# Optimization experiments

Measured on AMD Instinct MI355X. Metric: run time of the kernel, lower is better.

The kernel has to match this reference:

```python
import jax, jax.numpy as jnp
import numpy as np

N = 20000        # nodes
E = 320000       # edges (avg degree 16)
F_IN = 128       # node_features
F2 = 64          # second_features (per-head out dim, LSTM hidden)
H = 8            # heads
D1 = H * F2      # 512, concat output of GATConv / LSTM input
NEG_SLOPE = 0.2  # GATConv default leaky_relu slope


def _gat_conv(x, src, dst, W, att_src, att_dst, bias):
    """PyG GATConv (concat=True, self-loops added, eval-mode dropout)."""
    n = x.shape[0]
    h = (x @ W).reshape(n, H, -1)                      # [N,H,F]
    a_s = (h * att_src).sum(-1)                        # [N,H]
    a_d = (h * att_dst).sum(-1)                        # [N,H]
    e = jax.nn.leaky_relu(a_s[src] + a_d[dst], NEG_SLOPE)   # [E',H]
    m = jax.ops.segment_max(e, dst, num_segments=n)    # [N,H]
    m = jnp.where(jnp.isfinite(m), m, 0.0)
    ex = jnp.exp(e - m[dst])
    denom = jax.ops.segment_sum(ex, dst, num_segments=n)
    alpha = ex / (denom[dst] + 1e-16)                  # [E',H]
    msg = h[src] * alpha[:, :, None]                   # [E',H,F]
    out = jax.ops.segment_sum(msg, dst, num_segments=n)  # [N,H,F]
    return out.reshape(n, -1) + bias                   # [N,H*F]


def _lstm_step(x, W_ih, W_hh, b_ih, b_hh):
    """Single-timestep PyTorch LSTM with zero initial (h0, c0). x: [N,D1]."""
    h0 = jnp.zeros((x.shape[0], F2), x.dtype)
    gates = x @ W_ih.T + b_ih + h0 @ W_hh.T + b_hh     # [N,4*F2]
    i, f, g, o = jnp.split(gates, 4, axis=-1)
    c = jax.nn.sigmoid(f) * 0.0 + jax.nn.sigmoid(i) * jnp.tanh(g)
    h = jax.nn.sigmoid(o) * jnp.tanh(c)
    return h, (h, c)


def setup_inputs() -> dict:
    key = jax.random.key(0)
    ks = jax.random.split(key, 16)

    def glorot(k, shape, fan_in):
        return jax.random.normal(k, shape, jnp.float32) * (1.0 / np.sqrt(fan_in))

    return {
        "x": jax.random.normal(ks[0], (N, F_IN), jnp.float32),
        "edge_index": jax.random.randint(ks[1], (2, E), 0, N, jnp.int32),
        "edge_weight": jax.random.uniform(ks[2], (E,), jnp.float32),
        # GATConv 1: F_IN -> H*F2
        "W1": glorot(ks[3], (F_IN, H * F2), F_IN),
        "att_src1": glorot(ks[4], (H, F2), F2),
        "att_dst1": glorot(ks[5], (H, F2), F2),
        "bias1": jnp.zeros((H * F2,), jnp.float32),
        # LSTM: input D1 -> hidden F2
        "W_ih": glorot(ks[6], (4 * F2, D1), D1),
        "W_hh": glorot(ks[7], (4 * F2, F2), F2),
        "b_ih": jnp.zeros((4 * F2,), jnp.float32),
        "b_hh": jnp.zeros((4 * F2,), jnp.float32),
        # GATConv 2: F2 -> H*F2
        "W2": glorot(ks[8], (F2, H * F2), F2),
        "att_src2": glorot(ks[9], (H, F2), F2),
        "att_dst2": glorot(ks[10], (H, F2), F2),
        "bias2": jnp.zeros((H * F2,), jnp.float32),
    }


def reference(x, edge_index, edge_weight, W1, att_src1, att_dst1, bias1,
              W_ih, W_hh, b_ih, b_hh, W2, att_src2, att_dst2, bias2):
    # edge_weight is accepted but unused, matching the original forward.
    loops = jnp.arange(N, dtype=edge_index.dtype)
    src = jnp.concatenate([edge_index[0], loops])      # add self-loops (PyG default)
    dst = jnp.concatenate([edge_index[1], loops])

    h = _gat_conv(x, src, dst, W1, att_src1, att_dst1, bias1)   # [N,512]
    h, hidden2 = _lstm_step(h, W_ih, W_hh, b_ih, b_hh)          # [N,64]
    h = jax.nn.relu(h)
    h = _gat_conv(h, src, dst, W2, att_src2, att_dst2, bias2)   # [N,512]
    return jax.nn.softmax(h, axis=1)
```

## Files before the change

kernel.cpp:

```cpp
#include <hip/hip_runtime.h>
#include <math.h>
#include <stdint.h>


__global__ void count_kernel(const int* __restrict__ dst, int* __restrict__ deg, int E) {
  int i = blockIdx.x * 256 + threadIdx.x;
  if (i < E) atomicAdd(&deg[dst[i]], 1);
}

__global__ void scan_kernel(const int* __restrict__ deg, int* __restrict__ rowptr, int n) {
  __shared__ int buf[1024];
  const int tid = threadIdx.x;
  const int i0 = tid * 20;
  int v[20];
  int tsum = 0;
#pragma unroll
  for (int k = 0; k < 20; ++k) {
    int i = i0 + k;
    v[k] = (i < n) ? (deg[i] + 1) : 0;
    tsum += v[k];
  }
  int incl = tsum;
  buf[tid] = incl;
  __syncthreads();
  for (int s = 1; s < 1024; s <<= 1) {
    int t = (tid >= (unsigned)s) ? buf[tid - s] : 0;
    __syncthreads();
    incl += t;
    buf[tid] = incl;
    __syncthreads();
  }
  int excl = incl - tsum;
#pragma unroll
  for (int k = 0; k < 20; ++k) {
    int i = i0 + k;
    if (i < n) rowptr[i] = excl;
    excl += v[k];
  }
  if (tid == 1023) rowptr[n] = incl;
}

__global__ void scatter_kernel(const int* __restrict__ src, const int* __restrict__ dst,
                               const int* __restrict__ rowptr, int* __restrict__ wp,
                               int* __restrict__ col, int E, int n) {
  int i = blockIdx.x * 256 + threadIdx.x;
  if (i < E) {
    int d = dst[i];
    int p = rowptr[d] + atomicAdd(&wp[d], 1);
    col[p] = src[i];
  } else if (i < E + n) {
    int d = i - E;
    int p = rowptr[d] + atomicAdd(&wp[d], 1);
    col[p] = d;
  }
}


__device__ __forceinline__ uint16_t bf16r(float x) {
  uint32_t u = __float_as_uint(x);
  return (uint16_t)((u + 0x7FFFu + ((u >> 16) & 1u)) >> 16);
}
__device__ __forceinline__ void bfsplit(float x, uint16_t& h, uint16_t& l) {
  h = bf16r(x);
  float hf = __uint_as_float((uint32_t)h << 16);
  l = bf16r(x - hf);
}

using bf16x8 = __attribute__((ext_vector_type(8))) short;
using f32x4  = __attribute__((ext_vector_type(4))) float;


__global__ __launch_bounds__(256) void gemm_mfma(
    const float* __restrict__ A, const uint16_t* __restrict__ Bh,
    const uint16_t* __restrict__ Bl, float* __restrict__ C,
    const float* __restrict__ bias,
    int M, int K, int lda, int aZ, int bZ, int ldc, int cZ, int biasZ) {
  constexpr int BM = 128, BN = 64, BK = 64;
  __shared__ __align__(16) uint16_t sAh[BM * BK], sAl[BM * BK];
  __shared__ __align__(16) uint16_t sBh[BN * BK], sBl[BN * BK];
  const int z = blockIdx.z;
  A += (size_t)z * aZ;
  Bh += (size_t)z * bZ;
  Bl += (size_t)z * bZ;
  C += (size_t)z * cZ;
  const int tid = threadIdx.x;
  const int wid = tid >> 6, lane = tid & 63;
  const int bm = blockIdx.y * BM;
  const int bn = blockIdx.x * BN;
  const int fr = lane & 15;
  const int kg = lane >> 4;
  const int mbase = wid * 32;
  f32x4 acc[2][4] = {};

  for (int k0 = 0; k0 < K; k0 += BK) {
#pragma unroll
    for (int s = 0; s < 8; ++s) {
      int idx = tid + s * 256;
      int row = idx >> 4;
      int c4 = (idx & 15) * 4;
      float4 v = make_float4(0.f, 0.f, 0.f, 0.f);
      if (bm + row < M)
        v = *reinterpret_cast<const float4*>(A + (size_t)(bm + row) * lda + k0 + c4);
      ushort4 h, l;
      bfsplit(v.x, h.x, l.x); bfsplit(v.y, h.y, l.y);
      bfsplit(v.z, h.z, l.z); bfsplit(v.w, h.w, l.w);
      int off = (row * BK + c4) * 2;
      off ^= (row & 7) << 4;
      *reinterpret_cast<ushort4*>(reinterpret_cast<char*>(sAh) + off) = h;
      *reinterpret_cast<ushort4*>(reinterpret_cast<char*>(sAl) + off) = l;
    }
#pragma unroll
    for (int s = 0; s < 2; ++s) {
      int idx = tid + s * 256;
      int row = idx >> 3;
      int c8 = (idx & 7) * 8;
      uint4 vh = *reinterpret_cast<const uint4*>(Bh + (size_t)(bn + row) * K + k0 + c8);
      uint4 vl = *reinterpret_cast<const uint4*>(Bl + (size_t)(bn + row) * K + k0 + c8);
      int off = (row * BK + c8) * 2;
      off ^= (row & 7) << 4;
      *reinterpret_cast<uint4*>(reinterpret_cast<char*>(sBh) + off) = vh;
      *reinterpret_cast<uint4*>(reinterpret_cast<char*>(sBl) + off) = vl;
    }
    __syncthreads();
#pragma unroll
    for (int ks = 0; ks < 2; ++ks) {
      bf16x8 ah[2], al[2], bh[4], bl[4];
#pragma unroll
      for (int i = 0; i < 2; ++i) {
        int m = mbase + i * 16 + fr;
        int off = m * (BK * 2) + ks * 64 + kg * 16;
        off ^= (m & 7) << 4;
        ah[i] = *reinterpret_cast<const bf16x8*>(reinterpret_cast<const char*>(sAh) + off);
        al[i] = *reinterpret_cast<const bf16x8*>(reinterpret_cast<const char*>(sAl) + off);
      }
#pragma unroll
      for (int j = 0; j < 4; ++j) {
        int n = j * 16 + fr;
        int off = n * (BK * 2) + ks * 64 + kg * 16;
        off ^= (n & 7) << 4;
        bh[j] = *reinterpret_cast<const bf16x8*>(reinterpret_cast<const char*>(sBh) + off);
        bl[j] = *reinterpret_cast<const bf16x8*>(reinterpret_cast<const char*>(sBl) + off);
      }
#pragma unroll
      for (int i = 0; i < 2; ++i)
#pragma unroll
        for (int j = 0; j < 4; ++j) {
          acc[i][j] = __builtin_amdgcn_mfma_f32_16x16x32_bf16(ah[i], bh[j], acc[i][j], 0, 0, 0);
          acc[i][j] = __builtin_amdgcn_mfma_f32_16x16x32_bf16(al[i], bh[j], acc[i][j], 0, 0, 0);
          acc[i][j] = __builtin_amdgcn_mfma_f32_16x16x32_bf16(ah[i], bl[j], acc[i][j], 0, 0, 0);
        }
    }
    __syncthreads();
  }
  float bz[4];
#pragma unroll
  for (int j = 0; j < 4; ++j)
    bz[j] = bias ? bias[(size_t)z * biasZ + bn + j * 16 + fr] : 0.f;
#pragma unroll
  for (int i = 0; i < 2; ++i) {
    int mr = bm + mbase + i * 16 + kg * 4;
#pragma unroll
    for (int r = 0; r < 4; ++r) {
      int m = mr + r;
      if (m < M) {
#pragma unroll
        for (int j = 0; j < 4; ++j)
          C[(size_t)m * ldc + bn + j * 16 + fr] = acc[i][j][r] + bz[j];
      }
    }
  }
}


__global__ void prep_all_kernel(const float* __restrict__ W_ih, const float* __restrict__ b_ih,
                                const float* __restrict__ b_hh, const float* __restrict__ W1,
                                const float* __restrict__ as1, const float* __restrict__ ad1,
                                const float* __restrict__ W2, const float* __restrict__ as2,
                                const float* __restrict__ ad2,
                                int* __restrict__ degwp,
                                uint16_t* __restrict__ Wtbh, uint16_t* __restrict__ Wtbl,
                                uint16_t* __restrict__ Bt1h, uint16_t* __restrict__ Bt1l,
                                uint16_t* __restrict__ Bt2h, uint16_t* __restrict__ Bt2l,
                                float* __restrict__ bsum, float* __restrict__ watt1,
                                float* __restrict__ watt2, int n2) {
  int idx = blockIdx.x * 256 + threadIdx.x;
  if (idx < n2) {
    degwp[idx] = 0;
    return;
  }
  int t = idx - n2;
  if (t < 98304) {
    int jp = t >> 9, k = t & 511;
    int j = (jp < 64) ? jp : jp + 64;
    uint16_t h, l;
    bfsplit(W_ih[(size_t)j * 512 + k], h, l);
    Wtbh[t] = h; Wtbl[t] = l;
    return;
  }
  t -= 98304;
  if (t < 65536) {
    int n = t >> 7, k = t & 127;
    uint16_t h, l;
    bfsplit(W1[(size_t)k * 512 + n], h, l);
    Bt1h[t] = h; Bt1l[t] = l;
    return;
  }
  t -= 65536;
  if (t < 32768) {
    int n = t >> 6, k = t & 63;
    uint16_t h, l;
    bfsplit(W2[(size_t)k * 512 + n], h, l);
    Bt2h[t] = h; Bt2l[t] = l;
    return;
  }
  t -= 32768;
  if (t < 192) {
    int j = (t < 64) ? t : t + 64;
    bsum[t] = b_ih[j] + b_hh[j];
    return;
  }
  t -= 192;
  if (t < 2048) {
    int f = t >> 4, c = t & 15;
    int k = c & 7;
    const float* att = ((c < 8) ? as1 : ad1) + k * 64;
    const float* w = W1 + (size_t)f * 512 + k * 64;
    float s = 0.f;
#pragma unroll
    for (int j = 0; j < 64; ++j) s = fmaf(w[j], att[j], s);
    watt1[t] = s;
    return;
  }
  t -= 2048;
  if (t < 1024) {
    int f = t >> 4, c = t & 15;
    int k = c & 7;
    const float* att = ((c < 8) ? as2 : ad2) + k * 64;
    const float* w = W2 + (size_t)f * 512 + k * 64;
    float s = 0.f;
#pragma unroll
    for (int j = 0; j < 64; ++j) s = fmaf(w[j], att[j], s);
    watt2[t] = s;
  }
}


template <int F>
__global__ __launch_bounds__(256) void attcoef_kernel(
    const float* __restrict__ feat, const float* __restrict__ watt,
    float* __restrict__ a_s, float* __restrict__ a_d, int n) {
  __shared__ float rows[16 * F];
  __shared__ float wbuf[F * 16];
  const int n0 = blockIdx.x * 16;
  const int tid = threadIdx.x;
  if (n0 + 16 <= n) {
    const float4* g = reinterpret_cast<const float4*>(feat + (size_t)n0 * F);
    float4* l = reinterpret_cast<float4*>(rows);
    for (int i = tid; i < 16 * F / 4; i += 256) l[i] = g[i];
  } else {
    for (int i = tid; i < 16 * F; i += 256) {
      int r = i / F;
      rows[i] = (n0 + r < n) ? feat[(size_t)(n0 + r) * F + (i - r * F)] : 0.f;
    }
  }
  {
    const float4* g = reinterpret_cast<const float4*>(watt);
    float4* l = reinterpret_cast<float4*>(wbuf);
    for (int i = tid; i < F * 16 / 4; i += 256) l[i] = g[i];
  }
  __syncthreads();
  const int local = tid >> 4, c = tid & 15;
  float s = 0.f;
#pragma unroll 8
  for (int f = 0; f < F; ++f) s = fmaf(rows[local * F + f], wbuf[f * 16 + c], s);
  const int node = n0 + local;
  if (node < n) {
    if (c < 8) a_s[(size_t)node * 8 + c] = s;
    else       a_d[(size_t)node * 8 + (c - 8)] = s;
  }
}


template <int F>
__global__ __launch_bounds__(256) void gat_aggregate_wave(
    const float* __restrict__ feat, const float* __restrict__ a_s,
    const float* __restrict__ a_d, const int* __restrict__ rowptr,
    const int* __restrict__ col, float* __restrict__ agg, int n) {
  constexpr int F4 = F / 4;
  constexpr int HPG = (F == 128) ? 4 : 2;
  __shared__ float s_alpha[4][8][8];
  __shared__ int s_cols[4][8];
  const int wid = threadIdx.x >> 6;
  const int lane = threadIdx.x & 63;
  const int node = blockIdx.x * 4 + wid;
  if (node >= n) return;
  const int start = rowptr[node];
  const int deg = rowptr[node + 1] - start;
  const int j = lane >> 3;
  const int h = lane & 7;
  const float adh = a_d[(size_t)node * 8 + h];
  float den = 0.f;
  for (int e = j; e < deg; e += 8) {
    int s = col[start + e];
    float v = a_s[(size_t)s * 8 + h] + adh;
    v = (v > 0.f) ? v : 0.2f * v;
    den += __expf(v);
  }
  den += __shfl_xor(den, 8);
  den += __shfl_xor(den, 16);
  den += __shfl_xor(den, 32);
  const float inv = 1.f / (den + 1e-16f);
  const int f4 = lane & (F4 - 1);
  const int hbase = (lane / F4) * HPG;
  float4 acc0 = make_float4(0.f, 0.f, 0.f, 0.f);
  float4 acc1 = make_float4(0.f, 0.f, 0.f, 0.f);
  float4 acc2 = make_float4(0.f, 0.f, 0.f, 0.f);
  float4 acc3 = make_float4(0.f, 0.f, 0.f, 0.f);
  for (int c0 = 0; c0 < deg; c0 += 8) {
    float aval = 0.f;
    int sj = 0;
    if (c0 + j < deg) {
      sj = col[start + c0 + j];
      float v = a_s[(size_t)sj * 8 + h] + adh;
      v = (v > 0.f) ? v : 0.2f * v;
      aval = __expf(v) * inv;
    }
    s_alpha[wid][j][h] = aval;
    if (h == 0) s_cols[wid][j] = sj;
    __builtin_amdgcn_wave_barrier();
    const int ce = min(8, deg - c0);
    for (int e = 0; e < ce; ++e) {
      int s = s_cols[wid][e];
      float4 fv = *reinterpret_cast<const float4*>(feat + (size_t)s * F + f4 * 4);
      if constexpr (HPG == 4) {
        float4 al = *reinterpret_cast<const float4*>(&s_alpha[wid][e][hbase]);
        acc0.x = fmaf(al.x, fv.x, acc0.x); acc0.y = fmaf(al.x, fv.y, acc0.y);
        acc0.z = fmaf(al.x, fv.z, acc0.z); acc0.w = fmaf(al.x, fv.w, acc0.w);
        acc1.x = fmaf(al.y, fv.x, acc1.x); acc1.y = fmaf(al.y, fv.y, acc1.y);
        acc1.z = fmaf(al.y, fv.z, acc1.z); acc1.w = fmaf(al.y, fv.w, acc1.w);
        acc2.x = fmaf(al.z, fv.x, acc2.x); acc2.y = fmaf(al.z, fv.y, acc2.y);
        acc2.z = fmaf(al.z, fv.z, acc2.z); acc2.w = fmaf(al.z, fv.w, acc2.w);
        acc3.x = fmaf(al.w, fv.x, acc3.x); acc3.y = fmaf(al.w, fv.y, acc3.y);
        acc3.z = fmaf(al.w, fv.z, acc3.z); acc3.w = fmaf(al.w, fv.w, acc3.w);
      } else {
        float2 al = *reinterpret_cast<const float2*>(&s_alpha[wid][e][hbase]);
        acc0.x = fmaf(al.x, fv.x, acc0.x); acc0.y = fmaf(al.x, fv.y, acc0.y);
        acc0.z = fmaf(al.x, fv.z, acc0.z); acc0.w = fmaf(al.x, fv.w, acc0.w);
        acc1.x = fmaf(al.y, fv.x, acc1.x); acc1.y = fmaf(al.y, fv.y, acc1.y);
        acc1.z = fmaf(al.y, fv.z, acc1.z); acc1.w = fmaf(al.y, fv.w, acc1.w);
      }
    }
    __builtin_amdgcn_wave_barrier();
  }
  float* outp = agg + (size_t)node * 8 * F + (size_t)hbase * F + f4 * 4;
  *reinterpret_cast<float4*>(outp) = acc0;
  *reinterpret_cast<float4*>(outp + F) = acc1;
  if constexpr (HPG == 4) {
    *reinterpret_cast<float4*>(outp + 2 * F) = acc2;
    *reinterpret_cast<float4*>(outp + 3 * F) = acc3;
  }
}


__global__ __launch_bounds__(256) void lstm_act_attcoef_kernel(
    const float* __restrict__ gates, const float* __restrict__ bsum,
    const float* __restrict__ watt2, float* __restrict__ h2,
    float* __restrict__ a_s2, float* __restrict__ a_d2, int n) {
  __shared__ float h2t[4][64];
  __shared__ float wbuf[64 * 16];
  const int tid = threadIdx.x;
  reinterpret_cast<float4*>(wbuf)[tid] = reinterpret_cast<const float4*>(watt2)[tid];
  const int nl = tid >> 6, j = tid & 63;
  const int node = blockIdx.x * 4 + nl;
  float hv = 0.f;
  if (node < n) {
    const float* g0 = gates + (size_t)node * 192;
    float iv = g0[j] + bsum[j];
    float gv = g0[64 + j] + bsum[64 + j];
    float ov = g0[128 + j] + bsum[128 + j];
    float c = (1.f / (1.f + __expf(-iv))) * tanhf(gv);
    hv = fmaxf((1.f / (1.f + __expf(-ov))) * tanhf(c), 0.f);
    h2[(size_t)node * 64 + j] = hv;
  }
  h2t[nl][j] = hv;
  __syncthreads();
  if (j < 16 && node < n) {
    float s = 0.f;
#pragma unroll 16
    for (int f = 0; f < 64; ++f) s = fmaf(h2t[nl][f], wbuf[f * 16 + j], s);
    if (j < 8) a_s2[(size_t)node * 8 + j] = s;
    else       a_d2[(size_t)node * 8 + (j - 8)] = s;
  }
}


__global__ __launch_bounds__(256) void softmax512_wave(const float* __restrict__ in,
                                                       float* __restrict__ out, int n) {
  const int wid = threadIdx.x >> 6, lane = threadIdx.x & 63;
  const int node = blockIdx.x * 4 + wid;
  if (node >= n) return;
  const float4* ip = reinterpret_cast<const float4*>(in + (size_t)node * 512);
  float4 v0 = ip[lane];
  float4 v1 = ip[64 + lane];
  float m = fmaxf(fmaxf(fmaxf(v0.x, v0.y), fmaxf(v0.z, v0.w)),
                  fmaxf(fmaxf(v1.x, v1.y), fmaxf(v1.z, v1.w)));
#pragma unroll
  for (int d = 1; d < 64; d <<= 1) m = fmaxf(m, __shfl_xor(m, d));
  float4 e0, e1;
  e0.x = __expf(v0.x - m); e0.y = __expf(v0.y - m);
  e0.z = __expf(v0.z - m); e0.w = __expf(v0.w - m);
  e1.x = __expf(v1.x - m); e1.y = __expf(v1.y - m);
  e1.z = __expf(v1.z - m); e1.w = __expf(v1.w - m);
  float s = e0.x + e0.y + e0.z + e0.w + e1.x + e1.y + e1.z + e1.w;
#pragma unroll
  for (int d = 1; d < 64; d <<= 1) s += __shfl_xor(s, d);
  float inv = 1.f / s;
  e0.x *= inv; e0.y *= inv; e0.z *= inv; e0.w *= inv;
  e1.x *= inv; e1.y *= inv; e1.z *= inv; e1.w *= inv;
  float4* op = reinterpret_cast<float4*>(out + (size_t)node * 512);
  op[lane] = e0;
  op[64 + lane] = e1;
}


extern "C" void kernel_launch(void* const* d_in, const int* in_sizes, int n_in,
                              void* d_out, int out_size, void* d_ws, size_t ws_size,
                              hipStream_t stream) {
  const float* x      = (const float*)d_in[0];
  const int*   ei     = (const int*)d_in[1];
  const float* W1     = (const float*)d_in[3];
  const float* att_s1 = (const float*)d_in[4];
  const float* att_d1 = (const float*)d_in[5];
  const float* bias1  = (const float*)d_in[6];
  const float* W_ih   = (const float*)d_in[7];
  const float* b_ih   = (const float*)d_in[9];
  const float* b_hh   = (const float*)d_in[10];
  const float* W2     = (const float*)d_in[11];
  const float* att_s2 = (const float*)d_in[12];
  const float* att_d2 = (const float*)d_in[13];
  const float* bias2  = (const float*)d_in[14];
  float* out = (float*)d_out;

  const int N = in_sizes[0] / 128;
  const int E = in_sizes[1] / 2;
  const int* src = ei;
  const int* dst = ei + E;

  char* p = (char*)d_ws;
  auto alloc = [&](size_t bytes) {
    char* r = p;
    p += (bytes + 255) & ~(size_t)255;
    return r;
  };
  float* slotA = (float*)alloc((size_t)N * 1024 * 4);
  float* slotB = (float*)alloc((size_t)N * 512 * 4);
  float* a_s1 = (float*)alloc((size_t)N * 8 * 4);
  float* a_d1 = (float*)alloc((size_t)N * 8 * 4);
  float* a_s2 = (float*)alloc((size_t)N * 8 * 4);
  float* a_d2 = (float*)alloc((size_t)N * 8 * 4);
  float* watt1 = (float*)alloc(128 * 16 * 4);
  float* watt2 = (float*)alloc(64 * 16 * 4);
  uint16_t* Wtbh = (uint16_t*)alloc((size_t)192 * 512 * 2);
  uint16_t* Wtbl = (uint16_t*)alloc((size_t)192 * 512 * 2);
  uint16_t* Bt1h = (uint16_t*)alloc((size_t)512 * 128 * 2);
  uint16_t* Bt1l = (uint16_t*)alloc((size_t)512 * 128 * 2);
  uint16_t* Bt2h = (uint16_t*)alloc((size_t)512 * 64 * 2);
  uint16_t* Bt2l = (uint16_t*)alloc((size_t)512 * 64 * 2);
  float* bsum = (float*)alloc(192 * 4);
  int* deg    = (int*)alloc((size_t)2 * N * 4);
  int* wp     = deg + N;
  int* rowptr = (int*)alloc((size_t)(N + 1) * 4);
  int* col    = (int*)alloc((size_t)(E + N) * 4);

  float* agg1   = slotA;
  float* g1     = slotB;
  float* gates2 = slotA;
  float* h2     = slotA + (size_t)N * 384;
  float* agg2   = slotA + (size_t)N * 448;
  float* h3p    = slotB;

  {
    int total = 2 * N + 98304 + 65536 + 32768 + 192 + 2048 + 1024;
    prep_all_kernel<<<(total + 255) / 256, 256, 0, stream>>>(
        W_ih, b_ih, b_hh, W1, att_s1, att_d1, W2, att_s2, att_d2,
        deg, Wtbh, Wtbl, Bt1h, Bt1l, Bt2h, Bt2l, bsum, watt1, watt2, 2 * N);
  }

  count_kernel<<<(E + 255) / 256, 256, 0, stream>>>(dst, deg, E);
  scan_kernel<<<1, 1024, 0, stream>>>(deg, rowptr, N);
  scatter_kernel<<<(E + N + 255) / 256, 256, 0, stream>>>(src, dst, rowptr, wp, col, E, N);

  attcoef_kernel<128><<<(N + 15) / 16, 256, 0, stream>>>(x, watt1, a_s1, a_d1, N);
  gat_aggregate_wave<128><<<(N + 3) / 4, 256, 0, stream>>>(x, a_s1, a_d1, rowptr, col, agg1, N);
  {
    dim3 g(1, (N + 127) / 128, 8);
    gemm_mfma<<<g, 256, 0, stream>>>(agg1, Bt1h, Bt1l, g1, bias1,
                                     N, 128, 1024, 128, 64 * 128,
                                     512, 64, 64);
  }

  {
    dim3 g(3, (N + 127) / 128, 1);
    gemm_mfma<<<g, 256, 0, stream>>>(g1, Wtbh, Wtbl, gates2, nullptr,
                                     N, 512, 512, 0, 0, 192, 0, 0);
  }
  lstm_act_attcoef_kernel<<<(N + 3) / 4, 256, 0, stream>>>(gates2, bsum, watt2,
                                                           h2, a_s2, a_d2, N);

  gat_aggregate_wave<64><<<(N + 3) / 4, 256, 0, stream>>>(h2, a_s2, a_d2, rowptr, col, agg2, N);
  {
    dim3 g(1, (N + 127) / 128, 8);
    gemm_mfma<<<g, 256, 0, stream>>>(agg2, Bt2h, Bt2l, h3p, bias2,
                                     N, 64, 512, 64, 64 * 64,
                                     512, 64, 64);
  }
  softmax512_wave<<<(N + 3) / 4, 256, 0, stream>>>(h3p, out, N);
}
```

Baseline: 338.2 us.

## Pre-split GEMM operands into bf16 hi/lo in producers and prefetch tiles

Producers (GAT aggregation and the first GEMM epilogue) now write bf16 hi/lo split arrays directly, so the GEMM loads pre-split operands instead of converting fp32 in its load loop. The GEMM gains register-staged prefetching of the next K tile during MFMA compute. A BM template parameter lets the LSTM gate GEMM use 64-row tiles for more blocks. Memory traffic is unchanged in bytes (two bf16s per float), but conversion work moves out of the GEMM inner loop. The cost is extra registers and extra barriers.

```diff
diff --git a/kernel.cpp b/kernel.cpp
--- a/kernel.cpp
+++ b/kernel.cpp
@@ -65,68 +65,98 @@
   float hf = __uint_as_float((uint32_t)h << 16);
   l = bf16r(x - hf);
 }
+__device__ __forceinline__ void store4split(uint16_t* oh, uint16_t* ol, float4 v) {
+  ushort4 h, l;
+  bfsplit(v.x, h.x, l.x); bfsplit(v.y, h.y, l.y);
+  bfsplit(v.z, h.z, l.z); bfsplit(v.w, h.w, l.w);
+  *reinterpret_cast<ushort4*>(oh) = h;
+  *reinterpret_cast<ushort4*>(ol) = l;
+}
 
 using bf16x8 = __attribute__((ext_vector_type(8))) short;
 using f32x4  = __attribute__((ext_vector_type(4))) float;
 
 
+template <int BM, bool SPLIT_OUT>
 __global__ __launch_bounds__(256) void gemm_mfma(
-    const float* __restrict__ A, const uint16_t* __restrict__ Bh,
-    const uint16_t* __restrict__ Bl, float* __restrict__ C,
+    const uint16_t* __restrict__ Ah, const uint16_t* __restrict__ Al,
+    const uint16_t* __restrict__ Bh, const uint16_t* __restrict__ Bl,
+    float* __restrict__ C, uint16_t* __restrict__ Ch, uint16_t* __restrict__ Cl,
     const float* __restrict__ bias,
     int M, int K, int lda, int aZ, int bZ, int ldc, int cZ, int biasZ) {
-  constexpr int BM = 128, BN = 64, BK = 64;
+  constexpr int BN = 64, BK = 64;
+  constexpr int TMf = BM / 64;
+  constexpr int ACH = (BM * 8) / 256;
+  constexpr int BCH = 2;
   __shared__ __align__(16) uint16_t sAh[BM * BK], sAl[BM * BK];
   __shared__ __align__(16) uint16_t sBh[BN * BK], sBl[BN * BK];
   const int z = blockIdx.z;
-  A += (size_t)z * aZ;
-  Bh += (size_t)z * bZ;
-  Bl += (size_t)z * bZ;
-  C += (size_t)z * cZ;
+  Ah += (size_t)z * aZ; Al += (size_t)z * aZ;
+  Bh += (size_t)z * bZ; Bl += (size_t)z * bZ;
   const int tid = threadIdx.x;
   const int wid = tid >> 6, lane = tid & 63;
   const int bm = blockIdx.y * BM;
   const int bn = blockIdx.x * BN;
   const int fr = lane & 15;
   const int kg = lane >> 4;
-  const int mbase = wid * 32;
-  f32x4 acc[2][4] = {};
-
-  for (int k0 = 0; k0 < K; k0 += BK) {
-#pragma unroll
-    for (int s = 0; s < 8; ++s) {
+  const int mbase = wid * (BM / 4);
+  f32x4 acc[TMf][4] = {};
+
+  uint4 pah[ACH], pal[ACH], pbh[BCH], pbl[BCH];
+  const uint4 zero4 = {0u, 0u, 0u, 0u};
+
+  auto loadT = [&](int k0) {
+#pragma unroll
+    for (int s = 0; s < ACH; ++s) {
       int idx = tid + s * 256;
-      int row = idx >> 4;
-      int c4 = (idx & 15) * 4;
-      float4 v = make_float4(0.f, 0.f, 0.f, 0.f);
-      if (bm + row < M)
-        v = *reinterpret_cast<const float4*>(A + (size_t)(bm + row) * lda + k0 + c4);
-      ushort4 h, l;
-      bfsplit(v.x, h.x, l.x); bfsplit(v.y, h.y, l.y);
-      bfsplit(v.z, h.z, l.z); bfsplit(v.w, h.w, l.w);
-      int off = (row * BK + c4) * 2;
-      off ^= (row & 7) << 4;
-      *reinterpret_cast<ushort4*>(reinterpret_cast<char*>(sAh) + off) = h;
-      *reinterpret_cast<ushort4*>(reinterpret_cast<char*>(sAl) + off) = l;
-    }
-#pragma unroll
-    for (int s = 0; s < 2; ++s) {
+      int row = idx >> 3, c8 = (idx & 7) * 8;
+      if (bm + row < M) {
+        pah[s] = *reinterpret_cast<const uint4*>(Ah + (size_t)(bm + row) * lda + k0 + c8);
+        pal[s] = *reinterpret_cast<const uint4*>(Al + (size_t)(bm + row) * lda + k0 + c8);
+      } else {
+        pah[s] = zero4; pal[s] = zero4;
+      }
+    }
+#pragma unroll
+    for (int s = 0; s < BCH; ++s) {
       int idx = tid + s * 256;
-      int row = idx >> 3;
-      int c8 = (idx & 7) * 8;
-      uint4 vh = *reinterpret_cast<const uint4*>(Bh + (size_t)(bn + row) * K + k0 + c8);
-      uint4 vl = *reinterpret_cast<const uint4*>(Bl + (size_t)(bn + row) * K + k0 + c8);
+      int row = idx >> 3, c8 = (idx & 7) * 8;
+      pbh[s] = *reinterpret_cast<const uint4*>(Bh + (size_t)(bn + row) * K + k0 + c8);
+      pbl[s] = *reinterpret_cast<const uint4*>(Bl + (size_t)(bn + row) * K + k0 + c8);
+    }
+  };
+  auto storeT = [&]() {
+#pragma unroll
+    for (int s = 0; s < ACH; ++s) {
+      int idx = tid + s * 256;
+      int row = idx >> 3, c8 = (idx & 7) * 8;
       int off = (row * BK + c8) * 2;
       off ^= (row & 7) << 4;
-      *reinterpret_cast<uint4*>(reinterpret_cast<char*>(sBh) + off) = vh;
-      *reinterpret_cast<uint4*>(reinterpret_cast<char*>(sBl) + off) = vl;
-    }
-    __syncthreads();
+      *reinterpret_cast<uint4*>(reinterpret_cast<char*>(sAh) + off) = pah[s];
+      *reinterpret_cast<uint4*>(reinterpret_cast<char*>(sAl) + off) = pal[s];
+    }
+#pragma unroll
+    for (int s = 0; s < BCH; ++s) {
+      int idx = tid + s * 256;
+      int row = idx >> 3, c8 = (idx & 7) * 8;
+      int off = (row * BK + c8) * 2;
+      off ^= (row & 7) << 4;
+      *reinterpret_cast<uint4*>(reinterpret_cast<char*>(sBh) + off) = pbh[s];
+      *reinterpret_cast<uint4*>(reinterpret_cast<char*>(sBl) + off) = pbl[s];
+    }
+  };
+
+  loadT(0);
+  storeT();
+  __syncthreads();
+  for (int k0 = 0; k0 < K; k0 += BK) {
+    const bool more = (k0 + BK) < K;
+    if (more) loadT(k0 + BK);
 #pragma unroll
     for (int ks = 0; ks < 2; ++ks) {
-      bf16x8 ah[2], al[2], bh[4], bl[4];
-#pragma unroll
-      for (int i = 0; i < 2; ++i) {
+      bf16x8 ah[TMf], al[TMf], bh[4], bl[4];
+#pragma unroll
+      for (int i = 0; i < TMf; ++i) {
         int m = mbase + i * 16 + fr;
         int off = m * (BK * 2) + ks * 64 + kg * 16;
         off ^= (m & 7) << 4;
@@ -142,7 +172,7 @@
         bl[j] = *reinterpret_cast<const bf16x8*>(reinterpret_cast<const char*>(sBl) + off);
       }
 #pragma unroll
-      for (int i = 0; i < 2; ++i)
+      for (int i = 0; i < TMf; ++i)
 #pragma unroll
         for (int j = 0; j < 4; ++j) {
           acc[i][j] = __builtin_amdgcn_mfma_f32_16x16x32_bf16(ah[i], bh[j], acc[i][j], 0, 0, 0);
@@ -150,22 +180,41 @@
           acc[i][j] = __builtin_amdgcn_mfma_f32_16x16x32_bf16(ah[i], bl[j], acc[i][j], 0, 0, 0);
         }
     }
-    __syncthreads();
+    if (more) {
+      __syncthreads();
+      storeT();
+      __syncthreads();
+    }
   }
   float bz[4];
 #pragma unroll
   for (int j = 0; j < 4; ++j)
     bz[j] = bias ? bias[(size_t)z * biasZ + bn + j * 16 + fr] : 0.f;
-#pragma unroll
-  for (int i = 0; i < 2; ++i) {
+  if (SPLIT_OUT) {
+    Ch += (size_t)z * cZ;
+    Cl += (size_t)z * cZ;
+  } else {
+    C += (size_t)z * cZ;
+  }
+#pragma unroll
+  for (int i = 0; i < TMf; ++i) {
     int mr = bm + mbase + i * 16 + kg * 4;
 #pragma unroll
     for (int r = 0; r < 4; ++r) {
       int m = mr + r;
       if (m < M) {
 #pragma unroll
-        for (int j = 0; j < 4; ++j)
-          C[(size_t)m * ldc + bn + j * 16 + fr] = acc[i][j][r] + bz[j];
+        for (int j = 0; j < 4; ++j) {
+          float v = acc[i][j][r] + bz[j];
+          size_t o = (size_t)m * ldc + bn + j * 16 + fr;
+          if (SPLIT_OUT) {
+            uint16_t h, l;
+            bfsplit(v, h, l);
+            Ch[o] = h; Cl[o] = l;
+          } else {
+            C[o] = v;
+          }
+        }
       }
     }
   }
@@ -285,7 +334,8 @@
 __global__ __launch_bounds__(256) void gat_aggregate_wave(
     const float* __restrict__ feat, const float* __restrict__ a_s,
     const float* __restrict__ a_d, const int* __restrict__ rowptr,
-    const int* __restrict__ col, float* __restrict__ agg, int n) {
+    const int* __restrict__ col, uint16_t* __restrict__ aggH,
+    uint16_t* __restrict__ aggL, int n) {
   constexpr int F4 = F / 4;
   constexpr int HPG = (F == 128) ? 4 : 2;
   __shared__ float s_alpha[4][8][8];
@@ -352,12 +402,12 @@
     }
     __builtin_amdgcn_wave_barrier();
   }
-  float* outp = agg + (size_t)node * 8 * F + (size_t)hbase * F + f4 * 4;
-  *reinterpret_cast<float4*>(outp) = acc0;
-  *reinterpret_cast<float4*>(outp + F) = acc1;
+  size_t base = (size_t)node * 8 * F + (size_t)hbase * F + f4 * 4;
+  store4split(aggH + base, aggL + base, acc0);
+  store4split(aggH + base + F, aggL + base + F, acc1);
   if constexpr (HPG == 4) {
-    *reinterpret_cast<float4*>(outp + 2 * F) = acc2;
-    *reinterpret_cast<float4*>(outp + 3 * F) = acc3;
+    store4split(aggH + base + 2 * F, aggL + base + 2 * F, acc2);
+    store4split(aggH + base + 3 * F, aggL + base + 3 * F, acc3);
   }
 }
 
@@ -452,8 +502,8 @@
     p += (bytes + 255) & ~(size_t)255;
     return r;
   };
-  float* slotA = (float*)alloc((size_t)N * 1024 * 4);
-  float* slotB = (float*)alloc((size_t)N * 512 * 4);
+  char* slotA = alloc((size_t)N * 4096);
+  char* slotB = alloc((size_t)N * 2048);
   float* a_s1 = (float*)alloc((size_t)N * 8 * 4);
   float* a_d1 = (float*)alloc((size_t)N * 8 * 4);
   float* a_s2 = (float*)alloc((size_t)N * 8 * 4);
@@ -472,12 +522,15 @@
   int* rowptr = (int*)alloc((size_t)(N + 1) * 4);
   int* col    = (int*)alloc((size_t)(E + N) * 4);
 
-  float* agg1   = slotA;
-  float* g1     = slotB;
-  float* gates2 = slotA;
-  float* h2     = slotA + (size_t)N * 384;
-  float* agg2   = slotA + (size_t)N * 448;
-  float* h3p    = slotB;
+  uint16_t* agg1h = (uint16_t*)slotA;
+  uint16_t* agg1l = agg1h + (size_t)N * 1024;
+  float* gates2 = (float*)slotA;
+  float* h2 = (float*)(slotA + (size_t)N * 768);
+  uint16_t* agg2h = (uint16_t*)(slotA + (size_t)N * 1024);
+  uint16_t* agg2l = agg2h + (size_t)N * 512;
+  uint16_t* g1h = (uint16_t*)slotB;
+  uint16_t* g1l = g1h + (size_t)N * 512;
+  float* h3p = (float*)slotB;
 
   {
     int total = 2 * N + 98304 + 65536 + 32768 + 192 + 2048 + 1024;
@@ -491,28 +544,31 @@
   scatter_kernel<<<(E + N + 255) / 256, 256, 0, stream>>>(src, dst, rowptr, wp, col, E, N);
 
   attcoef_kernel<128><<<(N + 15) / 16, 256, 0, stream>>>(x, watt1, a_s1, a_d1, N);
-  gat_aggregate_wave<128><<<(N + 3) / 4, 256, 0, stream>>>(x, a_s1, a_d1, rowptr, col, agg1, N);
+  gat_aggregate_wave<128><<<(N + 3) / 4, 256, 0, stream>>>(x, a_s1, a_d1, rowptr, col,
+                                                           agg1h, agg1l, N);
   {
     dim3 g(1, (N + 127) / 128, 8);
-    gemm_mfma<<<g, 256, 0, stream>>>(agg1, Bt1h, Bt1l, g1, bias1,
-                                     N, 128, 1024, 128, 64 * 128,
-                                     512, 64, 64);
+    gemm_mfma<128, true><<<g, 256, 0, stream>>>(
+        agg1h, agg1l, Bt1h, Bt1l, nullptr, g1h, g1l, bias1,
+        N, 128, 1024, 128, 64 * 128, 512, 64, 64);
   }
 
   {
-    dim3 g(3, (N + 127) / 128, 1);
-    gemm_mfma<<<g, 256, 0, stream>>>(g1, Wtbh, Wtbl, gates2, nullptr,
-                                     N, 512, 512, 0, 0, 192, 0, 0);
+    dim3 g(3, (N + 63) / 64, 1);
+    gemm_mfma<64, false><<<g, 256, 0, stream>>>(
+        g1h, g1l, Wtbh, Wtbl, gates2, nullptr, nullptr, nullptr,
+        N, 512, 512, 0, 0, 192, 0, 0);
   }
   lstm_act_attcoef_kernel<<<(N + 3) / 4, 256, 0, stream>>>(gates2, bsum, watt2,
                                                            h2, a_s2, a_d2, N);
 
-  gat_aggregate_wave<64><<<(N + 3) / 4, 256, 0, stream>>>(h2, a_s2, a_d2, rowptr, col, agg2, N);
+  gat_aggregate_wave<64><<<(N + 3) / 4, 256, 0, stream>>>(h2, a_s2, a_d2, rowptr, col,
+                                                          agg2h, agg2l, N);
   {
     dim3 g(1, (N + 127) / 128, 8);
-    gemm_mfma<<<g, 256, 0, stream>>>(agg2, Bt2h, Bt2l, h3p, bias2,
-                                     N, 64, 512, 64, 64 * 64,
-                                     512, 64, 64);
+    gemm_mfma<128, false><<<g, 256, 0, stream>>>(
+        agg2h, agg2l, Bt2h, Bt2l, h3p, nullptr, nullptr, bias2,
+        N, 64, 512, 64, 64 * 64, 512, 64, 64);
   }
   softmax512_wave<<<(N + 3) / 4, 256, 0, stream>>>(h3p, out, N);
 }
```

Result: slower. 435.2 us (+28.7%).
